# Kernel tuning notes

Measured on AMD Instinct MI355X. Metric: run time of the kernel, lower is better.

The kernel has to match this reference:

```python
import jax, jax.numpy as jnp
import numpy as np

EMBED_DIM = 2048
NUM_HEADS = 16
LATENT_DIM = 512
HEAD_DIM = EMBED_DIM // NUM_HEADS


def setup_inputs() -> dict:
    key = jax.random.key(0)
    ks = jax.random.split(key, 9)
    s = 0.02
    x = jax.random.normal(ks[0], (2, 2048, EMBED_DIM), dtype=jnp.float32)
    # torch Linear weights stored as [out, in]
    q_w = jax.random.normal(ks[1], (EMBED_DIM, EMBED_DIM), jnp.float32) * s
    q_b = jax.random.normal(ks[2], (EMBED_DIM,), jnp.float32) * s
    kvd_w = jax.random.normal(ks[3], (LATENT_DIM, EMBED_DIM), jnp.float32) * s
    kvd_b = jax.random.normal(ks[4], (LATENT_DIM,), jnp.float32) * s
    kvu_w = jax.random.normal(ks[5], (EMBED_DIM * 2, LATENT_DIM), jnp.float32) * s
    kvu_b = jax.random.normal(ks[6], (EMBED_DIM * 2,), jnp.float32) * s
    out_w = jax.random.normal(ks[7], (EMBED_DIM, EMBED_DIM), jnp.float32) * s
    out_b = jax.random.normal(ks[8], (EMBED_DIM,), jnp.float32) * s
    return {"x": x, "q_w": q_w, "q_b": q_b, "kvd_w": kvd_w, "kvd_b": kvd_b,
            "kvu_w": kvu_w, "kvu_b": kvu_b, "out_w": out_w, "out_b": out_b}


def reference(x, q_w, q_b, kvd_w, kvd_b, kvu_w, kvu_b, out_w, out_b):
    b, s, _ = x.shape
    q = x @ q_w.T + q_b                      # [b,s,E]
    latent = x @ kvd_w.T + kvd_b             # [b,s,L]
    kv = latent @ kvu_w.T + kvu_b            # [b,s,2E]
    k, v = kv[..., :EMBED_DIM], kv[..., EMBED_DIM:]
    def heads(t):
        return t.reshape(b, s, NUM_HEADS, HEAD_DIM).transpose(0, 2, 1, 3)  # [b,h,s,d]
    qh, kh, vh = heads(q), heads(k), heads(v)
    scores = jnp.einsum('bhqd,bhkd->bhqk', qh, kh) / jnp.sqrt(jnp.float32(HEAD_DIM))
    attn = jax.nn.softmax(scores, axis=-1)
    out = jnp.einsum('bhqk,bhkd->bhqd', attn, vh)
    out = out.transpose(0, 2, 1, 3).reshape(b, s, EMBED_DIM)
    return out @ out_w.T + out_b
```

## Files before the change

kernel.cpp:

```cpp
#include <hip/hip_runtime.h>

typedef unsigned short u16;
typedef __attribute__((ext_vector_type(8))) __bf16 bf16x8;
typedef __attribute__((ext_vector_type(8))) unsigned short u16x8;
typedef __attribute__((ext_vector_type(4))) float f32x4;
typedef __attribute__((ext_vector_type(16))) float f32x16;

#define BK 32
#define TILE_ELEMS (128 * BK)

__device__ __forceinline__ u16 f32_to_bf16(float f) {
  unsigned int u = __builtin_bit_cast(unsigned int, f);
  u += 0x7fffu + ((u >> 16) & 1u);
  return (u16)(u >> 16);
}

__global__ __launch_bounds__(256) void cvt_bf16(const float* __restrict__ in,
                                                u16* __restrict__ out, int n) {
  int i = (blockIdx.x * 256 + threadIdx.x) * 4;
  if (i >= n) return;
  float4 v = *(const float4*)(in + i);
  ushort4 o;
  o.x = f32_to_bf16(v.x);
  o.y = f32_to_bf16(v.y);
  o.z = f32_to_bf16(v.z);
  o.w = f32_to_bf16(v.w);
  *(ushort4*)(out + i) = o;
}

__device__ __forceinline__ void gemm_core(const u16* __restrict__ A_tile,
                                          const u16* __restrict__ B_tile, int K,
                                          u16* As, u16* Bs, f32x4 acc[4][4]) {
  const int tid = threadIdx.x;
  const int w = tid >> 6, lane = tid & 63;
  const int wm = (w >> 1) << 6, wn = (w & 1) << 6;
  const int quad = lane >> 4, l15 = lane & 15;

  const u16* Ap = A_tile + (tid >> 2) * K + (tid & 3) * 8;
  const u16* Bp = B_tile + (tid >> 2) * K + (tid & 3) * 8;

  u16x8 ra0 = *(const u16x8*)Ap;
  u16x8 ra1 = *(const u16x8*)(Ap + 64 * K);
  u16x8 rb0 = *(const u16x8*)Bp;
  u16x8 rb1 = *(const u16x8*)(Bp + 64 * K);
  *(u16x8*)(As + tid * 8) = ra0;
  *(u16x8*)(As + (256 + tid) * 8) = ra1;
  *(u16x8*)(Bs + tid * 8) = rb0;
  *(u16x8*)(Bs + (256 + tid) * 8) = rb1;

  int p = 0;
  for (int k0 = 0; k0 < K; k0 += BK) {
    const int kn = (k0 + BK < K) ? (k0 + BK) : 0;
    ra0 = *(const u16x8*)(Ap + kn);
    ra1 = *(const u16x8*)(Ap + 64 * K + kn);
    rb0 = *(const u16x8*)(Bp + kn);
    rb1 = *(const u16x8*)(Bp + 64 * K + kn);
    __syncthreads();
    const u16* Asr = As + p * TILE_ELEMS;
    const u16* Bsr = Bs + p * TILE_ELEMS;
    bf16x8 af[4], bf[4];
#pragma unroll
    for (int i = 0; i < 4; i++)
      af[i] = *(const bf16x8*)(Asr + (wm + i * 16 + l15) * BK + quad * 8);
#pragma unroll
    for (int j = 0; j < 4; j++)
      bf[j] = *(const bf16x8*)(Bsr + (wn + j * 16 + l15) * BK + quad * 8);
#pragma unroll
    for (int i = 0; i < 4; i++)
#pragma unroll
      for (int j = 0; j < 4; j++)
        acc[i][j] =
            __builtin_amdgcn_mfma_f32_16x16x32_bf16(af[i], bf[j], acc[i][j], 0, 0, 0);
    const int pn = p ^ 1;
    u16* Asw = As + pn * TILE_ELEMS;
    u16* Bsw = Bs + pn * TILE_ELEMS;
    *(u16x8*)(Asw + tid * 8) = ra0;
    *(u16x8*)(Asw + (256 + tid) * 8) = ra1;
    *(u16x8*)(Bsw + tid * 8) = rb0;
    *(u16x8*)(Bsw + (256 + tid) * 8) = rb1;
    p = pn;
  }
}

__global__ __launch_bounds__(256) void gemm_qlat(const u16* __restrict__ X,
                                                 const u16* __restrict__ QW,
                                                 const u16* __restrict__ KVDW,
                                                 const float* __restrict__ q_b,
                                                 const float* __restrict__ kvd_b,
                                                 u16* __restrict__ Qb,
                                                 u16* __restrict__ Lat) {
  __shared__ __align__(16) u16 As[2 * TILE_ELEMS];
  __shared__ __align__(16) u16 Bs[2 * TILE_ELEMS];
  const int bn = blockIdx.x, bm = blockIdx.y;
  const bool isq = bn < 16;
  const u16* B_tile = isq ? QW + (size_t)bn * 128 * 2048
                          : KVDW + (size_t)(bn - 16) * 128 * 2048;
  f32x4 acc[4][4];
  const f32x4 z = {0.f, 0.f, 0.f, 0.f};
#pragma unroll
  for (int i = 0; i < 4; i++)
#pragma unroll
    for (int j = 0; j < 4; j++) acc[i][j] = z;
  gemm_core(X + (size_t)bm * 128 * 2048, B_tile, 2048, As, Bs, acc);

  const float* bias = isq ? q_b : kvd_b;
  u16* C = isq ? Qb : Lat;
  const int N = isq ? 2048 : 512;
  const int colbase = (isq ? bn : bn - 16) * 128;

  const int tid = threadIdx.x;
  const int w = tid >> 6, lane = tid & 63;
  const int wm = (w >> 1) << 6, wn = (w & 1) << 6;
  const int quad = lane >> 4, l15 = lane & 15;
  const int row0 = bm * 128 + wm + quad * 4;
  const int col0 = colbase + wn + l15;
#pragma unroll
  for (int i = 0; i < 4; i++)
#pragma unroll
    for (int j = 0; j < 4; j++) {
      int col = col0 + j * 16;
      float bv = bias[col];
#pragma unroll
      for (int r = 0; r < 4; r++) {
        int row = row0 + i * 16 + r;
        C[(size_t)row * N + col] = f32_to_bf16(acc[i][j][r] + bv);
      }
    }
}

__global__ __launch_bounds__(256) void gemm_f32out(const u16* __restrict__ A,
                                                   const u16* __restrict__ B,
                                                   const float* __restrict__ bias,
                                                   float* __restrict__ C, int K, int N) {
  __shared__ __align__(16) u16 As[2 * TILE_ELEMS];
  __shared__ __align__(16) u16 Bs[2 * TILE_ELEMS];
  f32x4 acc[4][4];
  const f32x4 z = {0.f, 0.f, 0.f, 0.f};
#pragma unroll
  for (int i = 0; i < 4; i++)
#pragma unroll
    for (int j = 0; j < 4; j++) acc[i][j] = z;
  gemm_core(A + (size_t)blockIdx.y * 128 * K, B + (size_t)blockIdx.x * 128 * K, K,
            As, Bs, acc);

  const int tid = threadIdx.x;
  const int w = tid >> 6, lane = tid & 63;
  const int wm = (w >> 1) << 6, wn = (w & 1) << 6;
  const int quad = lane >> 4, l15 = lane & 15;
  const int row0 = blockIdx.y * 128 + wm + quad * 4;
  const int col0 = blockIdx.x * 128 + wn + l15;
#pragma unroll
  for (int i = 0; i < 4; i++)
#pragma unroll
    for (int j = 0; j < 4; j++) {
      int col = col0 + j * 16;
      float bv = bias[col];
#pragma unroll
      for (int r = 0; r < 4; r++) {
        int row = row0 + i * 16 + r;
        C[(size_t)row * N + col] = acc[i][j][r] + bv;
      }
    }
}

__global__ __launch_bounds__(256) void gemm_kv(const u16* __restrict__ A,
                                               const u16* __restrict__ B,
                                               const float* __restrict__ bias,
                                               u16* __restrict__ Khat,
                                               u16* __restrict__ Vt, int K) {
  __shared__ __align__(16) u16 As[2 * TILE_ELEMS];
  __shared__ __align__(16) u16 Bs[2 * TILE_ELEMS];
  f32x4 acc[4][4];
  const f32x4 z = {0.f, 0.f, 0.f, 0.f};
#pragma unroll
  for (int i = 0; i < 4; i++)
#pragma unroll
    for (int j = 0; j < 4; j++) acc[i][j] = z;
  gemm_core(A + (size_t)blockIdx.y * 128 * K, B + (size_t)blockIdx.x * 128 * K, K,
            As, Bs, acc);

  const int tid = threadIdx.x;
  const int w = tid >> 6, lane = tid & 63;
  const int wm = (w >> 1) << 6, wn = (w & 1) << 6;
  const int quad = lane >> 4, l15 = lane & 15;
  const int row0 = blockIdx.y * 128 + wm + quad * 4;
  const int col0 = blockIdx.x * 128 + wn + l15;
#pragma unroll
  for (int i = 0; i < 4; i++)
#pragma unroll
    for (int j = 0; j < 4; j++) {
      int n = col0 + j * 16;
      float bv = bias[n];
#pragma unroll
      for (int r = 0; r < 4; r++) {
        int row = row0 + i * 16 + r;
        int bb = row >> 11, s = row & 2047;
        u16 val = f32_to_bf16(acc[i][j][r] + bv);
        if (n < 2048) {
          int h = n >> 7, d = n & 127;
          Khat[((size_t)(bb * 16 + h) * 2048 + s) * 128 + d] = val;
        } else {
          int h = (n - 2048) >> 7, d = n & 127;
          Vt[((size_t)(bb * 16 + h) * 128 + d) * 2048 + s] = val;
        }
      }
    }
}

__global__ __launch_bounds__(256) void attn_kernel(const u16* __restrict__ Q,
                                                   const u16* __restrict__ Khat,
                                                   const u16* __restrict__ Vt,
                                                   u16* __restrict__ O) {
  __shared__ __align__(16) u16 Ks[2][32 * 136];
  __shared__ __align__(16) u16 Vs[2][128 * 40];
  __shared__ __align__(16) u16 Ps[4 * 32 * 40];

  const int tid = threadIdx.x;
  const int w = tid >> 6, lane = tid & 63;
  const int l31 = lane & 31, half = lane >> 5;
  const int qt = blockIdx.x & 15;
  const int h = (blockIdx.x >> 4) & 15;
  const int b = blockIdx.x >> 8;
  const int bh = b * 16 + h;
  const float SC = 0.08838834764831845f * 1.4426950408889634f;

  bf16x8 qf[8];
  {
    const u16* qrow = Q + (size_t)(b * 2048 + qt * 128 + w * 32 + l31) * 2048 +
                      h * 128 + half * 8;
#pragma unroll
    for (int kc = 0; kc < 8; kc++) qf[kc] = *(const bf16x8*)(qrow + kc * 16);
  }

  f32x16 oacc[4];
#pragma unroll
  for (int nt = 0; nt < 4; nt++)
#pragma unroll
    for (int r = 0; r < 16; r++) oacc[nt][r] = 0.f;
  float lsum[16];
#pragma unroll
  for (int r = 0; r < 16; r++) lsum[r] = 0.f;

  const u16* Kg = Khat + (size_t)bh * 2048 * 128;
  const u16* Vg = Vt + (size_t)bh * 128 * 2048;
  u16* Pw = Ps + w * 32 * 40;

  const int kkr = tid >> 4, kc0 = tid & 15;
  const int vd = tid >> 2, vc0 = tid & 3;

  u16x8 kv[2], vv[2];
#pragma unroll
  for (int it = 0; it < 2; it++) {
    kv[it] = *(const u16x8*)(Kg + (size_t)(kkr + it * 16) * 128 + kc0 * 8);
    vv[it] = *(const u16x8*)(Vg + (size_t)(vd + it * 64) * 2048 + vc0 * 8);
  }
#pragma unroll
  for (int it = 0; it < 2; it++) {
    *(u16x8*)(Ks[0] + (kkr + it * 16) * 136 + kc0 * 8) = kv[it];
    *(u16x8*)(Vs[0] + (vd + it * 64) * 40 + vc0 * 8) = vv[it];
  }

  int p = 0;
  for (int key0 = 0; key0 < 2048; key0 += 32) {
    const int kn = (key0 + 32 < 2048) ? (key0 + 32) : 0;
#pragma unroll
    for (int it = 0; it < 2; it++) {
      kv[it] = *(const u16x8*)(Kg + (size_t)(kn + kkr + it * 16) * 128 + kc0 * 8);
      vv[it] = *(const u16x8*)(Vg + (size_t)(vd + it * 64) * 2048 + kn + vc0 * 8);
    }
    __syncthreads();

    f32x16 sacc;
#pragma unroll
    for (int r = 0; r < 16; r++) sacc[r] = 0.f;
#pragma unroll
    for (int kc = 0; kc < 8; kc++) {
      bf16x8 kf = *(const bf16x8*)(Ks[p] + l31 * 136 + kc * 16 + half * 8);
      sacc = __builtin_amdgcn_mfma_f32_32x32x16_bf16(qf[kc], kf, sacc, 0, 0, 0);
    }

#pragma unroll
    for (int r = 0; r < 16; r++) {
      float e = exp2f(sacc[r] * SC);
      lsum[r] += e;
      int ridx = (r & 3) + 8 * (r >> 2) + 4 * half;
      Pw[ridx * 40 + l31] = f32_to_bf16(e);
    }

    bf16x8 pf[2];
#pragma unroll
    for (int kc = 0; kc < 2; kc++)
      pf[kc] = *(const bf16x8*)(Pw + l31 * 40 + kc * 16 + half * 8);
#pragma unroll
    for (int nt = 0; nt < 4; nt++)
#pragma unroll
      for (int kc = 0; kc < 2; kc++) {
        bf16x8 vf = *(const bf16x8*)(Vs[p] + (nt * 32 + l31) * 40 + kc * 16 + half * 8);
        oacc[nt] = __builtin_amdgcn_mfma_f32_32x32x16_bf16(pf[kc], vf, oacc[nt], 0, 0, 0);
      }

    const int pn = p ^ 1;
#pragma unroll
    for (int it = 0; it < 2; it++) {
      *(u16x8*)(Ks[pn] + (kkr + it * 16) * 136 + kc0 * 8) = kv[it];
      *(u16x8*)(Vs[pn] + (vd + it * 64) * 40 + vc0 * 8) = vv[it];
    }
    p = pn;
  }

#pragma unroll
  for (int r = 0; r < 16; r++) {
    float s = lsum[r];
    s += __shfl_xor(s, 1);
    s += __shfl_xor(s, 2);
    s += __shfl_xor(s, 4);
    s += __shfl_xor(s, 8);
    s += __shfl_xor(s, 16);
    lsum[r] = 1.0f / s;
  }

#pragma unroll
  for (int nt = 0; nt < 4; nt++)
#pragma unroll
    for (int r = 0; r < 16; r++) {
      int ridx = (r & 3) + 8 * (r >> 2) + 4 * half;
      int row = b * 2048 + qt * 128 + w * 32 + ridx;
      int col = h * 128 + nt * 32 + l31;
      O[(size_t)row * 2048 + col] = f32_to_bf16(oacc[nt][r] * lsum[r]);
    }
}

extern "C" void kernel_launch(void* const* d_in, const int* in_sizes, int n_in,
                              void* d_out, int out_size, void* d_ws, size_t ws_size,
                              hipStream_t stream) {
  (void)in_sizes; (void)n_in; (void)out_size; (void)ws_size;
  const float* x     = (const float*)d_in[0];
  const float* q_w   = (const float*)d_in[1];
  const float* q_b   = (const float*)d_in[2];
  const float* kvd_w = (const float*)d_in[3];
  const float* kvd_b = (const float*)d_in[4];
  const float* kvu_w = (const float*)d_in[5];
  const float* kvu_b = (const float*)d_in[6];
  const float* out_w = (const float*)d_in[7];
  const float* out_b = (const float*)d_in[8];
  float* out = (float*)d_out;

  char* p = (char*)d_ws;
  u16* X    = (u16*)(p + 0);
  u16* W1   = (u16*)(p + (size_t)16 * 1024 * 1024);
  u16* W2   = (u16*)(p + (size_t)24 * 1024 * 1024);
  u16* Qb   = (u16*)(p + (size_t)26 * 1024 * 1024);
  u16* Lat  = (u16*)(p + (size_t)42 * 1024 * 1024);
  u16* Khat = (u16*)(p + (size_t)46 * 1024 * 1024);
  u16* Vt   = (u16*)(p + (size_t)62 * 1024 * 1024);
  u16* AO   = (u16*)(p + (size_t)78 * 1024 * 1024);

  cvt_bf16<<<dim3(8192), dim3(256), 0, stream>>>(x, X, 8388608);
  cvt_bf16<<<dim3(4096), dim3(256), 0, stream>>>(q_w, W1, 4194304);
  cvt_bf16<<<dim3(1024), dim3(256), 0, stream>>>(kvd_w, W2, 1048576);

  gemm_qlat<<<dim3(20, 32), dim3(256), 0, stream>>>(X, W1, W2, q_b, kvd_b, Qb, Lat);

  cvt_bf16<<<dim3(2048), dim3(256), 0, stream>>>(kvu_w, W1, 2097152);
  gemm_kv<<<dim3(32, 32), dim3(256), 0, stream>>>(Lat, W1, kvu_b, Khat, Vt, 512);

  cvt_bf16<<<dim3(4096), dim3(256), 0, stream>>>(out_w, X, 4194304);
  attn_kernel<<<dim3(512), dim3(256), 0, stream>>>(Qb, Khat, Vt, AO);
  gemm_f32out<<<dim3(16, 32), dim3(256), 0, stream>>>(AO, X, out_b, out, 2048, 2048);
}
```

Measured before the change: 415.7 us.

## Keep attention probabilities in registers via transposed QK MFMA and merge conversions

The QK^T MFMA now has its operands swapped, so each lane holds scores for one query and its exponentials can be packed straight into bf16 MFMA A-operands. This removes the per-tile LDS round trip for P. V is stored into LDS with a permuted key order to match that register layout. The softmax scale and log2(e) factor are folded into Q in the projection epilogue. The row sum becomes one scalar per lane with a single cross-half shuffle. The five fp32-to-bf16 conversion launches are merged into one kernel writing separate buffers, which drops launches and serialization at the cost of a larger workspace.

```diff
diff --git a/kernel.cpp b/kernel.cpp
--- a/kernel.cpp
+++ b/kernel.cpp
@@ -8,6 +8,7 @@
 
 #define BK 32
 #define TILE_ELEMS (128 * BK)
+#define QSCALE 0.12753706518066536f
 
 __device__ __forceinline__ u16 f32_to_bf16(float f) {
   unsigned int u = __builtin_bit_cast(unsigned int, f);
@@ -15,17 +16,32 @@
   return (u16)(u >> 16);
 }
 
-__global__ __launch_bounds__(256) void cvt_bf16(const float* __restrict__ in,
-                                                u16* __restrict__ out, int n) {
-  int i = (blockIdx.x * 256 + threadIdx.x) * 4;
-  if (i >= n) return;
-  float4 v = *(const float4*)(in + i);
+__device__ __forceinline__ unsigned int pack_bf16(float a, float b) {
+  return (unsigned int)f32_to_bf16(a) | ((unsigned int)f32_to_bf16(b) << 16);
+}
+
+__global__ __launch_bounds__(256) void cvt_all(
+    const float* __restrict__ x, const float* __restrict__ qw,
+    const float* __restrict__ kvdw, const float* __restrict__ kvuw,
+    const float* __restrict__ outw, u16* __restrict__ X, u16* __restrict__ W1,
+    u16* __restrict__ W2, u16* __restrict__ W3, u16* __restrict__ W4) {
+  int blk = blockIdx.x;
+  const float* src;
+  u16* dst;
+  int base;
+  if (blk < 8192)       { src = x;    dst = X;  base = blk; }
+  else if (blk < 12288) { src = qw;   dst = W1; base = blk - 8192; }
+  else if (blk < 13312) { src = kvdw; dst = W2; base = blk - 12288; }
+  else if (blk < 15360) { src = kvuw; dst = W3; base = blk - 13312; }
+  else                  { src = outw; dst = W4; base = blk - 15360; }
+  int i = base * 1024 + threadIdx.x * 4;
+  float4 v = *(const float4*)(src + i);
   ushort4 o;
   o.x = f32_to_bf16(v.x);
   o.y = f32_to_bf16(v.y);
   o.z = f32_to_bf16(v.z);
   o.w = f32_to_bf16(v.w);
-  *(ushort4*)(out + i) = o;
+  *(ushort4*)(dst + i) = o;
 }
 
 __device__ __forceinline__ void gemm_core(const u16* __restrict__ A_tile,
@@ -106,6 +122,7 @@
   const float* bias = isq ? q_b : kvd_b;
   u16* C = isq ? Qb : Lat;
   const int N = isq ? 2048 : 512;
+  const float scale = isq ? QSCALE : 1.0f;
   const int colbase = (isq ? bn : bn - 16) * 128;
 
   const int tid = threadIdx.x;
@@ -123,7 +140,7 @@
 #pragma unroll
       for (int r = 0; r < 4; r++) {
         int row = row0 + i * 16 + r;
-        C[(size_t)row * N + col] = f32_to_bf16(acc[i][j][r] + bv);
+        C[(size_t)row * N + col] = f32_to_bf16((acc[i][j][r] + bv) * scale);
       }
     }
 }
@@ -213,7 +230,6 @@
                                                    u16* __restrict__ O) {
   __shared__ __align__(16) u16 Ks[2][32 * 136];
   __shared__ __align__(16) u16 Vs[2][128 * 40];
-  __shared__ __align__(16) u16 Ps[4 * 32 * 40];
 
   const int tid = threadIdx.x;
   const int w = tid >> 6, lane = tid & 63;
@@ -222,7 +238,6 @@
   const int h = (blockIdx.x >> 4) & 15;
   const int b = blockIdx.x >> 8;
   const int bh = b * 16 + h;
-  const float SC = 0.08838834764831845f * 1.4426950408889634f;
 
   bf16x8 qf[8];
   {
@@ -237,16 +252,15 @@
   for (int nt = 0; nt < 4; nt++)
 #pragma unroll
     for (int r = 0; r < 16; r++) oacc[nt][r] = 0.f;
-  float lsum[16];
-#pragma unroll
-  for (int r = 0; r < 16; r++) lsum[r] = 0.f;
+  float lsum = 0.f;
 
   const u16* Kg = Khat + (size_t)bh * 2048 * 128;
   const u16* Vg = Vt + (size_t)bh * 128 * 2048;
-  u16* Pw = Ps + w * 32 * 40;
 
   const int kkr = tid >> 4, kc0 = tid & 15;
   const int vd = tid >> 2, vc0 = tid & 3;
+  const int vlo = (vc0 >> 1) * 16 + (vc0 & 1) * 4;
+  const int vhi = vlo + 8;
 
   u16x8 kv[2], vv[2];
 #pragma unroll
@@ -257,7 +271,9 @@
 #pragma unroll
   for (int it = 0; it < 2; it++) {
     *(u16x8*)(Ks[0] + (kkr + it * 16) * 136 + kc0 * 8) = kv[it];
-    *(u16x8*)(Vs[0] + (vd + it * 64) * 40 + vc0 * 8) = vv[it];
+    const unsigned long long* vp = (const unsigned long long*)&vv[it];
+    *(unsigned long long*)(Vs[0] + (vd + it * 64) * 40 + vlo) = vp[0];
+    *(unsigned long long*)(Vs[0] + (vd + it * 64) * 40 + vhi) = vp[1];
   }
 
   int p = 0;
@@ -276,47 +292,48 @@
 #pragma unroll
     for (int kc = 0; kc < 8; kc++) {
       bf16x8 kf = *(const bf16x8*)(Ks[p] + l31 * 136 + kc * 16 + half * 8);
-      sacc = __builtin_amdgcn_mfma_f32_32x32x16_bf16(qf[kc], kf, sacc, 0, 0, 0);
-    }
-
+      sacc = __builtin_amdgcn_mfma_f32_32x32x16_bf16(kf, qf[kc], sacc, 0, 0, 0);
+    }
+
+    float e[16];
 #pragma unroll
     for (int r = 0; r < 16; r++) {
-      float e = exp2f(sacc[r] * SC);
-      lsum[r] += e;
-      int ridx = (r & 3) + 8 * (r >> 2) + 4 * half;
-      Pw[ridx * 40 + l31] = f32_to_bf16(e);
-    }
-
-    bf16x8 pf[2];
-#pragma unroll
-    for (int kc = 0; kc < 2; kc++)
-      pf[kc] = *(const bf16x8*)(Pw + l31 * 40 + kc * 16 + half * 8);
-#pragma unroll
-    for (int nt = 0; nt < 4; nt++)
-#pragma unroll
-      for (int kc = 0; kc < 2; kc++) {
-        bf16x8 vf = *(const bf16x8*)(Vs[p] + (nt * 32 + l31) * 40 + kc * 16 + half * 8);
-        oacc[nt] = __builtin_amdgcn_mfma_f32_32x32x16_bf16(pf[kc], vf, oacc[nt], 0, 0, 0);
-      }
+      e[r] = exp2f(sacc[r]);
+      lsum += e[r];
+    }
+    union { unsigned int u[4]; bf16x8 v; } p0, p1;
+#pragma unroll
+    for (int i = 0; i < 4; i++) {
+      p0.u[i] = pack_bf16(e[2 * i], e[2 * i + 1]);
+      p1.u[i] = pack_bf16(e[8 + 2 * i], e[9 + 2 * i]);
+    }
+
+#pragma unroll
+    for (int nt = 0; nt < 4; nt++) {
+      bf16x8 vf0 = *(const bf16x8*)(Vs[p] + (nt * 32 + l31) * 40 + half * 8);
+      bf16x8 vf1 = *(const bf16x8*)(Vs[p] + (nt * 32 + l31) * 40 + 16 + half * 8);
+      oacc[nt] = __builtin_amdgcn_mfma_f32_32x32x16_bf16(p0.v, vf0, oacc[nt], 0, 0, 0);
+      oacc[nt] = __builtin_amdgcn_mfma_f32_32x32x16_bf16(p1.v, vf1, oacc[nt], 0, 0, 0);
+    }
 
     const int pn = p ^ 1;
 #pragma unroll
     for (int it = 0; it < 2; it++) {
       *(u16x8*)(Ks[pn] + (kkr + it * 16) * 136 + kc0 * 8) = kv[it];
-      *(u16x8*)(Vs[pn] + (vd + it * 64) * 40 + vc0 * 8) = vv[it];
+      const unsigned long long* vp = (const unsigned long long*)&vv[it];
+      *(unsigned long long*)(Vs[pn] + (vd + it * 64) * 40 + vlo) = vp[0];
+      *(unsigned long long*)(Vs[pn] + (vd + it * 64) * 40 + vhi) = vp[1];
     }
     p = pn;
   }
 
+  lsum += __shfl_xor(lsum, 32);
+  float inv = 1.0f / lsum;
+  float wr[16];
 #pragma unroll
   for (int r = 0; r < 16; r++) {
-    float s = lsum[r];
-    s += __shfl_xor(s, 1);
-    s += __shfl_xor(s, 2);
-    s += __shfl_xor(s, 4);
-    s += __shfl_xor(s, 8);
-    s += __shfl_xor(s, 16);
-    lsum[r] = 1.0f / s;
+    int ridx = (r & 3) + 8 * (r >> 2) + 4 * half;
+    wr[r] = __shfl(inv, ridx);
   }
 
 #pragma unroll
@@ -326,7 +343,7 @@
       int ridx = (r & 3) + 8 * (r >> 2) + 4 * half;
       int row = b * 2048 + qt * 128 + w * 32 + ridx;
       int col = h * 128 + nt * 32 + l31;
-      O[(size_t)row * 2048 + col] = f32_to_bf16(oacc[nt][r] * lsum[r]);
+      O[(size_t)row * 2048 + col] = f32_to_bf16(oacc[nt][r] * wr[r]);
     }
 }
 
@@ -349,22 +366,18 @@
   u16* X    = (u16*)(p + 0);
   u16* W1   = (u16*)(p + (size_t)16 * 1024 * 1024);
   u16* W2   = (u16*)(p + (size_t)24 * 1024 * 1024);
-  u16* Qb   = (u16*)(p + (size_t)26 * 1024 * 1024);
-  u16* Lat  = (u16*)(p + (size_t)42 * 1024 * 1024);
-  u16* Khat = (u16*)(p + (size_t)46 * 1024 * 1024);
-  u16* Vt   = (u16*)(p + (size_t)62 * 1024 * 1024);
-  u16* AO   = (u16*)(p + (size_t)78 * 1024 * 1024);
-
-  cvt_bf16<<<dim3(8192), dim3(256), 0, stream>>>(x, X, 8388608);
-  cvt_bf16<<<dim3(4096), dim3(256), 0, stream>>>(q_w, W1, 4194304);
-  cvt_bf16<<<dim3(1024), dim3(256), 0, stream>>>(kvd_w, W2, 1048576);
-
+  u16* W3   = (u16*)(p + (size_t)26 * 1024 * 1024);
+  u16* W4   = (u16*)(p + (size_t)30 * 1024 * 1024);
+  u16* Qb   = (u16*)(p + (size_t)38 * 1024 * 1024);
+  u16* Lat  = (u16*)(p + (size_t)54 * 1024 * 1024);
+  u16* Khat = (u16*)(p + (size_t)58 * 1024 * 1024);
+  u16* Vt   = (u16*)(p + (size_t)74 * 1024 * 1024);
+  u16* AO   = (u16*)(p + (size_t)90 * 1024 * 1024);
+
+  cvt_all<<<dim3(19456), dim3(256), 0, stream>>>(x, q_w, kvd_w, kvu_w, out_w,
+                                                 X, W1, W2, W3, W4);
   gemm_qlat<<<dim3(20, 32), dim3(256), 0, stream>>>(X, W1, W2, q_b, kvd_b, Qb, Lat);
-
-  cvt_bf16<<<dim3(2048), dim3(256), 0, stream>>>(kvu_w, W1, 2097152);
-  gemm_kv<<<dim3(32, 32), dim3(256), 0, stream>>>(Lat, W1, kvu_b, Khat, Vt, 512);
-
-  cvt_bf16<<<dim3(4096), dim3(256), 0, stream>>>(out_w, X, 4194304);
+  gemm_kv<<<dim3(32, 32), dim3(256), 0, stream>>>(Lat, W3, kvu_b, Khat, Vt, 512);
   attn_kernel<<<dim3(512), dim3(256), 0, stream>>>(Qb, Khat, Vt, AO);
-  gemm_f32out<<<dim3(16, 32), dim3(256), 0, stream>>>(AO, X, out_b, out, 2048, 2048);
-}
+  gemm_f32out<<<dim3(16, 32), dim3(256), 0, stream>>>(AO, W4, out_b, out, 2048, 2048);
+}
```

Measured after the change: 386.7 us. -7.0%, faster.
